# Optimization experiments

Hardware: AMD Instinct MI355X
Metric: run time of the kernel (lower is better)

## Reference

```python
import jax, jax.numpy as jnp
import numpy as np

EPS = 1e-5


def _bn_relu(y, g, beta, relu=True):
    # BatchNorm1d in training mode: biased batch stats over (B, V) per channel
    mean = jnp.mean(y, axis=(0, 2), keepdims=True)
    var = jnp.mean((y - mean) ** 2, axis=(0, 2), keepdims=True)
    out = (y - mean) * jax.lax.rsqrt(var + EPS) * g[None, :, None] + beta[None, :, None]
    return jnp.maximum(out, 0.0) if relu else out


def _spiral_conv(x, idx, w, b, g, beta):
    # x: (B,C,V), idx: (V,L) -> gather (B,C,V,L), row-major reshape to (B,C*L,V)
    B, C, V = x.shape
    L = idx.shape[1]
    neigh = x[:, :, idx].reshape(B, C * L, V)
    y = jnp.einsum('om,bmv->bov', w, neigh) + b[None, :, None]
    return _bn_relu(y, g, beta)


def _se(x, w1, w2):
    s = jnp.mean(x, axis=2)                              # (B,C)
    h = jnp.maximum(jnp.einsum('bc,rc->br', s, w1), 0.0)  # (B,r)
    s = jax.nn.sigmoid(jnp.einsum('br,cr->bc', h, w2))   # (B,C)
    return x * s[:, :, None]


def setup_inputs() -> dict:
    key = jax.random.key(0)
    ks = jax.random.split(key, 24)
    B, V, L, H = 2, 16384, 12, 256
    sc = 0.05
    inp = {
        'verts': jax.random.normal(ks[0], (B, V, 3), jnp.float32),
        'spirals': jax.random.randint(ks[1], (4, V, L), 0, V, jnp.int32),
        'enc0_w': jax.random.normal(ks[2], (H, 3 * L), jnp.float32) * sc,
        'enc0_b': jax.random.normal(ks[3], (H,), jnp.float32) * sc,
        'enc0_g': jnp.ones((H,), jnp.float32),
        'enc0_beta': jnp.zeros((H,), jnp.float32),
        'enc_w': jax.random.normal(ks[4], (3, H, H * L), jnp.float32) * sc,
        'enc_b': jax.random.normal(ks[5], (3, H), jnp.float32) * sc,
        'enc_g': jnp.ones((3, H), jnp.float32),
        'enc_beta': jnp.zeros((3, H), jnp.float32),
        'se_w1': jax.random.normal(ks[6], (4, H // 8, H), jnp.float32) * sc,
        'se_w2': jax.random.normal(ks[7], (4, H, H // 8), jnp.float32) * sc,
        'skip_w': jax.random.normal(ks[8], (3, H, 2 * H), jnp.float32) * sc,
        'skip_b': jax.random.normal(ks[9], (3, H), jnp.float32) * sc,
        'dec_w': jax.random.normal(ks[10], (3, H, H * L), jnp.float32) * sc,
        'dec_b': jax.random.normal(ks[11], (3, H), jnp.float32) * sc,
        'dec_g': jnp.ones((3, H), jnp.float32),
        'dec_beta': jnp.zeros((3, H), jnp.float32),
        'cls1_w': jax.random.normal(ks[12], (H // 2, H), jnp.float32) * sc,
        'cls1_b': jax.random.normal(ks[13], (H // 2,), jnp.float32) * sc,
        'cls1_g': jnp.ones((H // 2,), jnp.float32),
        'cls1_beta': jnp.zeros((H // 2,), jnp.float32),
        'cls2_w': jax.random.normal(ks[14], (H // 4, H // 2), jnp.float32) * sc,
        'cls2_b': jax.random.normal(ks[15], (H // 4,), jnp.float32) * sc,
        'cls2_g': jnp.ones((H // 4,), jnp.float32),
        'cls2_beta': jnp.zeros((H // 4,), jnp.float32),
        'cls3_w': jax.random.normal(ks[16], (1, H // 4), jnp.float32) * sc,
        'cls3_b': jax.random.normal(ks[17], (1,), jnp.float32) * sc,
    }
    return inp


def reference(verts, spirals, enc0_w, enc0_b, enc0_g, enc0_beta,
              enc_w, enc_b, enc_g, enc_beta, se_w1, se_w2,
              skip_w, skip_b, dec_w, dec_b, dec_g, dec_beta,
              cls1_w, cls1_b, cls1_g, cls1_beta,
              cls2_w, cls2_b, cls2_g, cls2_beta, cls3_w, cls3_b):
    x = jnp.transpose(verts, (0, 2, 1))  # (B,3,V)
    feats = []
    # encoder: 4 blocks, block0 has no residual (3 != 256)
    for i in range(4):
        if i == 0:
            out = _spiral_conv(x, spirals[0], enc0_w, enc0_b, enc0_g, enc0_beta)
        else:
            out = _spiral_conv(x, spirals[i], enc_w[i - 1], enc_b[i - 1], enc_g[i - 1], enc_beta[i - 1]) + x
        x = _se(out, se_w1[i], se_w2[i])
        feats.append(x)
    # decoder with skip-concat fusion, spirals[2],[1],[0] and feats[2],[1],[0]
    for i in range(3):
        feat = feats[2 - i]
        idx = spirals[2 - i]
        xc = jnp.concatenate([x, feat], axis=1)  # (B,512,V)
        x = jnp.einsum('oc,bcv->bov', skip_w[i], xc) + skip_b[i][None, :, None]
        x = _spiral_conv(x, idx, dec_w[i], dec_b[i], dec_g[i], dec_beta[i]) + x
    # classifier: 1x1 conv stack
    h = _bn_relu(jnp.einsum('oc,bcv->bov', cls1_w, x) + cls1_b[None, :, None], cls1_g, cls1_beta)
    h = _bn_relu(jnp.einsum('oc,bcv->bov', cls2_w, h) + cls2_b[None, :, None], cls2_g, cls2_beta)
    out = jnp.einsum('oc,bcv->bov', cls3_w, h) + cls3_b[None, :, None]  # (B,1,V)
    return out[:, 0, :]  # (B,V)
```

## Files before the change

kernel.cpp:

```cpp
#include <hip/hip_runtime.h>

typedef unsigned short u16;
using f16x8 = __attribute__((ext_vector_type(8))) _Float16;
using f32x4 = __attribute__((ext_vector_type(4))) float;

#define V_N 16384
#define M_N 32768

__device__ __forceinline__ float h2f(u16 u) {
  _Float16 h; __builtin_memcpy(&h, &u, 2); return (float)h;
}
__device__ __forceinline__ u16 f2h(float f) {
  _Float16 h = (_Float16)f; u16 u; __builtin_memcpy(&u, &h, 2); return u;
}

__device__ __forceinline__ void dma16(const u16* g, u16* l) {
  __builtin_amdgcn_global_load_lds(
      (const __attribute__((address_space(1))) void*)(const void*)g,
      (__attribute__((address_space(3))) void*)(void*)l, 16, 0, 0);
}

__device__ __forceinline__ void d_perm2(int bid, const float* __restrict__ w, u16* __restrict__ wp) {
  int o = bid & 255, layer = bid >> 8;
  int t = threadIdx.x;
  const float* src = w + ((size_t)layer * 256 + o) * 3072;
  u16* dst = wp + (size_t)layer * 786432;
  float2 v[6];
  #pragma unroll
  for (int q = 0; q < 6; ++q) v[q] = *(const float2*)(src + t * 12 + q * 2);
  const float* vf = (const float*)v;
  int lo = t & 31;
  #pragma unroll
  for (int m = 0; m < 12; ++m) {
    int kc = m * 8 + (t >> 5);
    dst[(size_t)kc * 8192 + o * 32 + lo] = f2h(vf[m]);
  }
}

__device__ __forceinline__ void d_permfr(int bid, const float* __restrict__ src, u16* __restrict__ dst,
                                         int O, int K) {
  int i = bid * 256 + threadIdx.x;
  if (i >= (K << 8)) return;
  int j = i & 7, lq = (i >> 3) & 3, col = (i >> 5) & 255, kc = i >> 13;
  int k = kc * 32 + lq * 8 + j;
  float v = (col < O) ? src[(size_t)col * K + k] : 0.f;
  dst[i] = f2h(v);
}

__global__ __launch_bounds__(256) void prep_k(
    const float* __restrict__ enc_w, const float* __restrict__ dec_w,
    const float* __restrict__ skip_w, const float* __restrict__ cls1_w,
    const float* __restrict__ cls2_w,
    u16* __restrict__ wpe, u16* __restrict__ wpe_dec, u16* __restrict__ skip_wb,
    u16* __restrict__ cls1_wb, u16* __restrict__ wp6, float* __restrict__ zbase)
{
  int b = blockIdx.x;
  if (b < 768) { d_perm2(b, enc_w, wpe); return; }
  b -= 768;
  if (b < 768) { d_perm2(b, dec_w, wpe_dec); return; }
  b -= 768;
  if (b < 1536) {
    int s = b >> 9, r = b & 511;
    d_permfr(r, skip_w + (size_t)s * 256 * 512, skip_wb + (size_t)s * 256 * 512, 256, 512);
    return;
  }
  b -= 1536;
  if (b < 256) { d_permfr(b, cls1_w, cls1_wb, 128, 256); return; }
  b -= 256;
  if (b < 128) { d_permfr(b, cls2_w, wp6, 64, 128); return; }
  b -= 128;
  int idx = (b * 256 + threadIdx.x) * 2;
  if (idx < 7168) { zbase[idx] = 0.f; zbase[idx + 1] = 0.f; }
}

__global__ __launch_bounds__(256) void wscale_k(const u16* __restrict__ w, const float* __restrict__ sig,
                                                const float* __restrict__ sigx,
                                                u16* __restrict__ o, int n, int sel) {
  int i = blockIdx.x * 256 + threadIdx.x;
  if (i >= n) return;
  float wv = h2f(w[i]);
  int k = (i >> 13) * 32 + ((i >> 3) & 3) * 8 + (i & 7);
  int c = k & 255;
  #pragma unroll
  for (int b = 0; b < 2; ++b) {
    float s;
    if (sel == 511 && k < 256) s = sigx ? sigx[b * 256 + c] : 1.f;
    else                       s = sig[b * 256 + c];
    o[(long)b * n + i] = f2h(wv * s);
  }
}

__global__ __launch_bounds__(256) void enc0_k(const float* __restrict__ verts, const int* __restrict__ sp,
                                              const float* __restrict__ w0, u16* __restrict__ y,
                                              float* __restrict__ st) {
  __shared__ float xs[32][36];
  int t = threadIdx.x;
  int r0 = blockIdx.x * 32;
  for (int s = t; s < 32 * 12; s += 256) {
    int row = s / 12, tt = s - row * 12;
    int gr = r0 + row;
    int b = gr >> 14, v = gr & (V_N - 1);
    int j = sp[tt * V_N + v];
    const float* p = verts + ((long)b * V_N + j) * 3;
    xs[row][tt]      = p[0];
    xs[row][12 + tt] = p[1];
    xs[row][24 + tt] = p[2];
  }
  __syncthreads();
  float w[36];
  #pragma unroll
  for (int k = 0; k < 36; ++k) w[k] = w0[t * 36 + k];
  float s1 = 0.f, s2 = 0.f;
  for (int row = 0; row < 32; ++row) {
    float a = 0.f;
    #pragma unroll
    for (int k = 0; k < 36; ++k) a += w[k] * xs[row][k];
    u16 h = f2h(a);
    y[(long)(r0 + row) * 256 + t] = h;
    float av = h2f(h);
    s1 += av; s2 += av * av;
  }
  atomicAdd(&st[t], s1);
  atomicAdd(&st[256 + t], s2);
}

template<int CT>
__global__ __launch_bounds__(512, 4) void gemm3_k(
    const u16* __restrict__ P0, const u16* __restrict__ P1, int lda,
    const int* __restrict__ sp, int L,
    const u16* __restrict__ Wt, long wstride,
    u16* __restrict__ Yb, const float* __restrict__ bias, int Ostore,
    float* __restrict__ stats)
{
  constexpr int KC   = CT >> 5;
  constexpr int PH   = (CT == 256) ? 4 : 2;
  constexpr int KCP  = KC / PH;
  constexpr int PROW = 64;
  constexpr int BUFE = 64 * PROW;
  __shared__ __align__(16) u16 lA[3 * BUFE];
  const int tid  = threadIdx.x;
  const int wave = tid >> 6, lane = tid & 63;
  const int wn = wave * 32;
  const int lr = lane & 15, lq = lane >> 4;
  const int nwg = gridDim.x;
  const int wg = (blockIdx.x & 7) * (nwg >> 3) + (blockIdx.x >> 3);
  const int bm = wg * 64;
  const int batch = bm >> 14;
  const int vbase = bm & (V_N - 1);
  const int qrow = lane >> 3;
  const int qchunk = lane & 7;
  const bool gat = (sp != nullptr);
  const long rowb = (long)batch * V_N;
  const u16* Pd1 = P1 ? P1 : P0;
  const u16* Wb = Wt + (long)batch * wstride;
  const int NS = PH * L;

  const u16* bp[2];
  #pragma unroll
  for (int nt = 0; nt < 2; ++nt)
    bp[nt] = Wb + ((long)(wn + nt * 16 + lr) * 4 + lq) * 8;

  const u16* aBase[4][2];
  #pragma unroll
  for (int mt = 0; mt < 4; ++mt)
    #pragma unroll
    for (int kp = 0; kp < 2; ++kp) {
      int row = mt * 16 + lr;
      aBase[mt][kp] = lA + row * PROW + (((kp * 4 + lq) ^ (row & 7)) << 3);
    }

  auto load_idx = [&](int tap) -> int {
    int v = 0;
    if (gat && lane < 8) v = sp[(long)tap * V_N + vbase + wave * 8 + lane];
    return v;
  };

  auto dma_st = [&](u16* buf, const u16* src, int idxreg, int ph) {
    u16* wb = buf + wave * (8 * PROW);
    int rloc = wave * 8 + qrow;
    long grow;
    if (gat) grow = rowb + (long)__shfl(idxreg, qrow, 64);
    else     grow = bm + rloc;
    const u16* gp = src + grow * lda + ph * PROW + ((qchunk ^ (rloc & 7)) << 3);
    dma16(gp, wb);
  };

  f32x4 acc[4][2];
  #pragma unroll
  for (int i = 0; i < 4; ++i)
    #pragma unroll
    for (int j = 0; j < 2; ++j) acc[i][j] = (f32x4){0.f, 0.f, 0.f, 0.f};

  f16x8 tA[KCP * 2], tB2[KCP * 2];

  auto adv = [&](int& l, int& ph) { if (++l == L) { l = 0; ++ph; } };
  int lB = 0, phB = 0; adv(lB, phB);
  int lD = lB, phD = phB; adv(lD, phD);
  int lI = lD; { int pT = phD; int lT = lI; adv(lT, pT); lI = lT; }
  int idxN;

  {
    int i0 = load_idx(0);
    int i1 = load_idx(lB);
    idxN = load_idx(lD);
    dma_st(lA, P0, i0, 0);
    if (NS > 1) {
      const u16* s1 = (!gat && lB > 0) ? Pd1 : P0;
      dma_st(lA + BUFE, s1, i1, phB);
    }
    __builtin_amdgcn_sched_barrier(0);
    #pragma unroll
    for (int kp = 0; kp < KCP; ++kp)
      #pragma unroll
      for (int nt = 0; nt < 2; ++nt)
        tA[kp * 2 + nt] = *(const f16x8*)(bp[nt] + (long)kp * 8192);
    __builtin_amdgcn_sched_barrier(0);
  }

  auto stage = [&](int s, f16x8 (&tCur)[KCP * 2], f16x8 (&tNxt)[KCP * 2]) {
    if (s + 1 < NS) asm volatile("s_waitcnt vmcnt(5)" ::: "memory");
    else            asm volatile("s_waitcnt vmcnt(0)" ::: "memory");
    asm volatile("s_waitcnt lgkmcnt(0)" ::: "memory");
    __builtin_amdgcn_s_barrier();
    __builtin_amdgcn_sched_barrier(0);
    const int so = (s % 3) * BUFE;
    const long cbB = (long)(lB * KC + phB * KCP);
    f16x8 a0[4];
    #pragma unroll
    for (int mt = 0; mt < 4; ++mt) a0[mt] = *(const f16x8*)(aBase[mt][0] + so);
    if (s + 1 < NS) {
      tNxt[0] = *(const f16x8*)(bp[0] + cbB * 8192);
      tNxt[1] = *(const f16x8*)(bp[1] + cbB * 8192);
    }
    __builtin_amdgcn_sched_barrier(0);
    __builtin_amdgcn_s_setprio(1);
    #pragma unroll
    for (int mt = 0; mt < 4; ++mt) {
      acc[mt][0] = __builtin_amdgcn_mfma_f32_16x16x32_f16(a0[mt], tCur[0], acc[mt][0], 0, 0, 0);
      acc[mt][1] = __builtin_amdgcn_mfma_f32_16x16x32_f16(a0[mt], tCur[1], acc[mt][1], 0, 0, 0);
    }
    __builtin_amdgcn_s_setprio(0);
    __builtin_amdgcn_sched_barrier(0);
    int idxT = 0;
    if (gat && s + 3 < NS) idxT = load_idx(lI);
    if (s + 2 < NS) {
      const u16* srcD = (!gat && lD > 0) ? Pd1 : P0;
      dma_st(lA + ((s + 2) % 3) * BUFE, srcD, idxN, phD);
    }
    __builtin_amdgcn_sched_barrier(0);
    f16x8 a1[4];
    #pragma unroll
    for (int mt = 0; mt < 4; ++mt) a1[mt] = *(const f16x8*)(aBase[mt][1] + so);
    if (s + 1 < NS) {
      tNxt[2] = *(const f16x8*)(bp[0] + (cbB + 1) * 8192);
      tNxt[3] = *(const f16x8*)(bp[1] + (cbB + 1) * 8192);
    }
    __builtin_amdgcn_sched_barrier(0);
    __builtin_amdgcn_s_setprio(1);
    #pragma unroll
    for (int mt = 0; mt < 4; ++mt) {
      acc[mt][0] = __builtin_amdgcn_mfma_f32_16x16x32_f16(a1[mt], tCur[2], acc[mt][0], 0, 0, 0);
      acc[mt][1] = __builtin_amdgcn_mfma_f32_16x16x32_f16(a1[mt], tCur[3], acc[mt][1], 0, 0, 0);
    }
    __builtin_amdgcn_s_setprio(0);
    adv(lB, phB); adv(lD, phD); if (++lI == L) lI = 0;
    idxN = idxT;
  };

  for (int s = 0; s < NS; s += 2) {
    stage(s, tA, tB2);
    stage(s + 1, tB2, tA);
  }

  #pragma unroll
  for (int nt = 0; nt < 2; ++nt) {
    int col = wn + nt * 16 + lr;
    if (col < Ostore) {
      float bv = bias ? bias[col] : 0.f;
      float s1 = 0.f, s2 = 0.f;
      #pragma unroll
      for (int mt = 0; mt < 4; ++mt) {
        #pragma unroll
        for (int rg = 0; rg < 4; ++rg) {
          int row = bm + mt * 16 + lq * 4 + rg;
          float v = acc[mt][nt][rg] + bv;
          Yb[(long)row * Ostore + col] = f2h(v);
          s1 += v; s2 += v * v;
        }
      }
      if (stats) {
        s1 += __shfl_xor(s1, 16); s1 += __shfl_xor(s1, 32);
        s2 += __shfl_xor(s2, 16); s2 += __shfl_xor(s2, 32);
        if (lq == 0) {
          atomicAdd(&stats[col], s1);
          atomicAdd(&stats[Ostore + col], s2);
        }
      }
    }
  }
}

__global__ __launch_bounds__(256) void bnrelu2_k(
    const u16* __restrict__ y, const float* __restrict__ st,
    const float* __restrict__ g, const float* __restrict__ be,
    const u16* __restrict__ resid, const float* __restrict__ rscale,
    u16* __restrict__ ob, float* __restrict__ ses, int O)
{
  __shared__ float sL[256];
  int tid = threadIdx.x;
  int tpr = O >> 2;
  int rpi = 256 / tpr;
  int ci = (tid & (tpr - 1)) * 4;
  int row0 = blockIdx.x * (rpi * 16);
  int r0 = row0 + (tid / tpr);
  int b = row0 >> 14;
  float mean[4], sc[4], sh[4], rs[4];
  #pragma unroll
  for (int j = 0; j < 4; ++j) {
    int c = ci + j;
    float m = st[c] * (1.f / 32768.f);
    float var = st[O + c] * (1.f / 32768.f) - m * m;
    mean[j] = m;
    sc[j] = rsqrtf(fmaxf(var, 0.f) + 1e-5f) * g[c];
    sh[j] = be[c];
    rs[j] = rscale ? rscale[b * 256 + c] : 1.f;
  }
  float ss[4] = {0,0,0,0};
  for (int it = 0; it < 16; ++it) {
    long i = ((long)r0 + (long)it * rpi) * O + ci;
    uint2 pv = *(const uint2*)(y + i);
    float v[4];
    v[0] = fmaxf((h2f((u16)(pv.x & 0xffff)) - mean[0]) * sc[0] + sh[0], 0.f);
    v[1] = fmaxf((h2f((u16)(pv.x >> 16))    - mean[1]) * sc[1] + sh[1], 0.f);
    v[2] = fmaxf((h2f((u16)(pv.y & 0xffff)) - mean[2]) * sc[2] + sh[2], 0.f);
    v[3] = fmaxf((h2f((u16)(pv.y >> 16))    - mean[3]) * sc[3] + sh[3], 0.f);
    if (resid) {
      uint2 rv = *(const uint2*)(resid + i);
      v[0] += h2f((u16)(rv.x & 0xffff)) * rs[0]; v[1] += h2f((u16)(rv.x >> 16)) * rs[1];
      v[2] += h2f((u16)(rv.y & 0xffff)) * rs[2]; v[3] += h2f((u16)(rv.y >> 16)) * rs[3];
    }
    uint2 pk;
    pk.x = (unsigned)f2h(v[0]) | ((unsigned)f2h(v[1]) << 16);
    pk.y = (unsigned)f2h(v[2]) | ((unsigned)f2h(v[3]) << 16);
    *(uint2*)(ob + i) = pk;
    #pragma unroll
    for (int j = 0; j < 4; ++j) ss[j] += v[j];
  }
  if (ses) {
    sL[tid] = 0.f;
    __syncthreads();
    #pragma unroll
    for (int j = 0; j < 4; ++j) atomicAdd(&sL[ci + j], ss[j]);
    __syncthreads();
    atomicAdd(&ses[b * O + tid], sL[tid]);
  }
}

__global__ void se_k(const float* __restrict__ ses, const float* __restrict__ w1,
                     const float* __restrict__ w2, float* __restrict__ sig)
{
  __shared__ float s[256];
  __shared__ float h[32];
  int b = blockIdx.x, t = threadIdx.x;
  s[t] = ses[b * 256 + t] * (1.f / 16384.f);
  __syncthreads();
  if (t < 32) {
    float a = 0.f;
    for (int c = 0; c < 256; ++c) a += w1[t * 256 + c] * s[c];
    h[t] = fmaxf(a, 0.f);
  }
  __syncthreads();
  float a = 0.f;
  #pragma unroll
  for (int r = 0; r < 32; ++r) a += w2[t * 32 + r] * h[r];
  sig[b * 256 + t] = 1.f / (1.f + expf(-a));
}

__global__ __launch_bounds__(256) void cls3_k(const u16* __restrict__ h2, const float* __restrict__ w,
                                              const float* __restrict__ b, float* __restrict__ out)
{
  __shared__ float ws[64];
  int t = threadIdx.x;
  if (t < 64) ws[t] = w[t];
  __syncthreads();
  int r = blockIdx.x * 256 + t;
  const u16* p = h2 + (long)r * 64;
  float a = b[0];
  #pragma unroll
  for (int c = 0; c < 64; ++c) a += ws[c] * h2f(p[c]);
  out[r] = a;
}

extern "C" void kernel_launch(void* const* d_in, const int* in_sizes, int n_in,
                              void* d_out, int out_size, void* d_ws, size_t ws_size,
                              hipStream_t stream)
{
  (void)in_sizes; (void)n_in; (void)out_size; (void)ws_size;
  const float* verts   = (const float*)d_in[0];
  const int*   spirals = (const int*)d_in[1];
  const float* enc0_w  = (const float*)d_in[2];
  const float* enc0_g  = (const float*)d_in[4];
  const float* enc0_be = (const float*)d_in[5];
  const float* enc_w   = (const float*)d_in[6];
  const float* enc_g   = (const float*)d_in[8];
  const float* enc_be  = (const float*)d_in[9];
  const float* se_w1   = (const float*)d_in[10];
  const float* se_w2   = (const float*)d_in[11];
  const float* skip_w  = (const float*)d_in[12];
  const float* skip_b  = (const float*)d_in[13];
  const float* dec_w   = (const float*)d_in[14];
  const float* dec_g   = (const float*)d_in[16];
  const float* dec_be  = (const float*)d_in[17];
  const float* cls1_w  = (const float*)d_in[18];
  const float* cls1_g  = (const float*)d_in[20];
  const float* cls1_be = (const float*)d_in[21];
  const float* cls2_w  = (const float*)d_in[22];
  const float* cls2_g  = (const float*)d_in[24];
  const float* cls2_be = (const float*)d_in[25];
  const float* cls3_w  = (const float*)d_in[26];
  const float* cls3_b  = (const float*)d_in[27];

  char* p = (char*)d_ws;
  auto alloc = [&](size_t n) { char* q = p; p += (n + 255) & ~(size_t)255; return q; };
  u16* wpe     = (u16*)alloc((size_t)6 * 256 * 3072 * 2);
  u16* wpe_s   = (u16*)alloc((size_t)3 * 2 * 256 * 3072 * 2);
  u16* skip_wb = (u16*)alloc((size_t)3 * 256 * 512 * 2);
  u16* skip_s  = (u16*)alloc((size_t)3 * 2 * 256 * 512 * 2);
  u16* cls1_wb = (u16*)alloc((size_t)256 * 256 * 2);
  u16* wp6     = (u16*)alloc((size_t)256 * 128 * 2);
  float* stats = (float*)alloc(10 * 2048);
  float* sesum = (float*)alloc(4 * 2048);
  float* sig   = (float*)alloc(4 * 2048);
  u16* out0 = (u16*)alloc((size_t)M_N * 256 * 2);
  u16* out1 = (u16*)alloc((size_t)M_N * 256 * 2);
  u16* out2 = (u16*)alloc((size_t)M_N * 256 * 2);
  u16* ct   = (u16*)alloc((size_t)M_N * 256 * 2);
  u16* tb   = (u16*)alloc((size_t)M_N * 256 * 2);
  u16* xd   = (u16*)alloc((size_t)M_N * 256 * 2);
  u16* outs[4] = {out0, out1, out2, ct};
  const size_t WENC = (size_t)256 * 3072;
  const size_t WSKP = (size_t)256 * 512;

  prep_k<<<3472, 256, 0, stream>>>(enc_w, dec_w, skip_w, cls1_w, cls2_w,
                                   wpe, wpe + (size_t)3 * WENC, skip_wb, cls1_wb, wp6,
                                   stats);

  enc0_k<<<1024, 256, 0, stream>>>(verts, spirals, enc0_w, ct, stats);
  bnrelu2_k<<<512, 256, 0, stream>>>(ct, stats, enc0_g, enc0_be, nullptr, nullptr, out0, sesum, 256);
  se_k<<<2, 256, 0, stream>>>(sesum, se_w1, se_w2, sig);

  for (int i = 1; i < 4; ++i) {
    wscale_k<<<3072, 256, 0, stream>>>(wpe + (size_t)(i - 1) * WENC, sig + (i - 1) * 512, nullptr,
                                       wpe_s + (size_t)(i - 1) * 2 * WENC, (int)WENC, 255);
    gemm3_k<256><<<512, 512, 0, stream>>>(outs[i - 1], nullptr, 256,
                                          spirals + (size_t)i * V_N * 12, 12,
                                          wpe_s + (size_t)(i - 1) * 2 * WENC, (long)WENC,
                                          ct, nullptr, 256, stats + i * 512);
    bnrelu2_k<<<512, 256, 0, stream>>>(ct, stats + i * 512, enc_g + (i - 1) * 256, enc_be + (i - 1) * 256,
                                       outs[i - 1], sig + (i - 1) * 512, outs[i], sesum + i * 512, 256);
    se_k<<<2, 256, 0, stream>>>(sesum + i * 512, se_w1 + (size_t)i * 32 * 256,
                                se_w2 + (size_t)i * 256 * 32, sig + i * 512);
  }

  for (int i = 0; i < 3; ++i) {
    wscale_k<<<512, 256, 0, stream>>>(skip_wb + (size_t)i * WSKP, sig + (2 - i) * 512,
                                      (i == 0) ? (sig + 3 * 512) : nullptr,
                                      skip_s + (size_t)i * 2 * WSKP, (int)WSKP, 511);
    gemm3_k<256><<<512, 512, 0, stream>>>((i == 0) ? ct : xd, outs[2 - i], 256, nullptr, 2,
                                          skip_s + (size_t)i * 2 * WSKP, (long)WSKP,
                                          tb, skip_b + i * 256, 256, nullptr);
    gemm3_k<256><<<512, 512, 0, stream>>>(tb, nullptr, 256,
                                          spirals + (size_t)(2 - i) * V_N * 12, 12,
                                          wpe + (size_t)(3 + i) * WENC, 0,
                                          outs[2 - i], nullptr, 256, stats + (4 + i) * 512);
    bnrelu2_k<<<512, 256, 0, stream>>>(outs[2 - i], stats + (4 + i) * 512, dec_g + i * 256, dec_be + i * 256,
                                       tb, nullptr, xd, nullptr, 256);
  }

  gemm3_k<256><<<512, 512, 0, stream>>>(xd, nullptr, 256, nullptr, 1,
                                        cls1_wb, 0, ct, nullptr, 128, stats + 7 * 512);
  bnrelu2_k<<<256, 256, 0, stream>>>(ct, stats + 7 * 512, cls1_g, cls1_be, nullptr, nullptr,
                                     ct, nullptr, 128);
  gemm3_k<128><<<512, 512, 0, stream>>>(ct, nullptr, 128, nullptr, 1,
                                        wp6, 0, tb, nullptr, 64, stats + 8 * 512);
  bnrelu2_k<<<128, 256, 0, stream>>>(tb, stats + 8 * 512, cls2_g, cls2_be, nullptr, nullptr,
                                     tb, nullptr, 64);
  cls3_k<<<128, 256, 0, stream>>>(tb, cls3_w, cls3_b, (float*)d_out);
}
```

Baseline: 868.6 us.

## Fold SE gate computation into consumers and fuse final classifier into BN kernel

Removes the standalone SE gate kernel and the final 1x1 classifier kernel. Each wscale and bnrelu block now recomputes the squeeze-excite gate from the channel sums in shared memory, and the last BN+ReLU pass does the 64-wide dot product with a shuffle reduction and writes the output directly. The aim is fewer launches and one less round trip of the hidden activations through memory. The cost is redundant gate work in every block: 3072 blocks for the encoder wscale each run a small MLP with several barriers, which could outweigh the launch savings.

Result: slower. 1.013 ms (+16.6%).

```diff
diff --git a/kernel.cpp b/kernel.cpp
--- a/kernel.cpp
+++ b/kernel.cpp
@@ -18,6 +18,36 @@
   __builtin_amdgcn_global_load_lds(
       (const __attribute__((address_space(1))) void*)(const void*)g,
       (__attribute__((address_space(3))) void*)(void*)l, 16, 0, 0);
+}
+
+__device__ __forceinline__ float gate256(const float* __restrict__ ses_b,
+                                         const float* __restrict__ w1,
+                                         const float* __restrict__ w2,
+                                         float* sL, float* h8, float* hL, int t)
+{
+  sL[t] = ses_b[t] * (1.f / 16384.f);
+  __syncthreads();
+  {
+    int r = t >> 3, gseg = t & 7;
+    const float* wr = w1 + r * 256 + gseg * 32;
+    const float* sv = sL + gseg * 32;
+    float a = 0.f;
+    #pragma unroll
+    for (int c = 0; c < 32; ++c) a += wr[c] * sv[c];
+    h8[t] = a;
+  }
+  __syncthreads();
+  if (t < 32) {
+    float a = 0.f;
+    #pragma unroll
+    for (int j = 0; j < 8; ++j) a += h8[t * 8 + j];
+    hL[t] = fmaxf(a, 0.f);
+  }
+  __syncthreads();
+  float a = 0.f;
+  #pragma unroll
+  for (int r = 0; r < 32; ++r) a += w2[t * 32 + r] * hL[r];
+  return 1.f / (1.f + expf(-a));
 }
 
 __device__ __forceinline__ void d_perm2(int bid, const float* __restrict__ w, u16* __restrict__ wp) {
@@ -73,19 +103,39 @@
   if (idx < 7168) { zbase[idx] = 0.f; zbase[idx + 1] = 0.f; }
 }
 
-__global__ __launch_bounds__(256) void wscale_k(const u16* __restrict__ w, const float* __restrict__ sig,
-                                                const float* __restrict__ sigx,
-                                                u16* __restrict__ o, int n, int sel) {
-  int i = blockIdx.x * 256 + threadIdx.x;
-  if (i >= n) return;
+__global__ __launch_bounds__(256) void wscale_k(
+    const u16* __restrict__ w,
+    const float* __restrict__ ses, const float* __restrict__ w1, const float* __restrict__ w2,
+    const float* __restrict__ sesx, const float* __restrict__ x1, const float* __restrict__ x2,
+    u16* __restrict__ o, int n, int sel)
+{
+  __shared__ float sL[256], h8[256], hL[32];
+  __shared__ float gA[512], gX[512];
+  int t = threadIdx.x;
+  #pragma unroll
+  for (int b = 0; b < 2; ++b) {
+    float v = gate256(ses + b * 256, w1, w2, sL, h8, hL, t);
+    __syncthreads();
+    gA[b * 256 + t] = v;
+  }
+  if (sesx) {
+    #pragma unroll
+    for (int b = 0; b < 2; ++b) {
+      float v = gate256(sesx + b * 256, x1, x2, sL, h8, hL, t);
+      __syncthreads();
+      gX[b * 256 + t] = v;
+    }
+  }
+  __syncthreads();
+  int i = blockIdx.x * 256 + t;
   float wv = h2f(w[i]);
   int k = (i >> 13) * 32 + ((i >> 3) & 3) * 8 + (i & 7);
   int c = k & 255;
   #pragma unroll
   for (int b = 0; b < 2; ++b) {
     float s;
-    if (sel == 511 && k < 256) s = sigx ? sigx[b * 256 + c] : 1.f;
-    else                       s = sig[b * 256 + c];
+    if (sel == 511 && k < 256) s = sesx ? gX[b * 256 + c] : 1.f;
+    else                       s = gA[b * 256 + c];
     o[(long)b * n + i] = f2h(wv * s);
   }
 }
@@ -303,10 +353,12 @@
 __global__ __launch_bounds__(256) void bnrelu2_k(
     const u16* __restrict__ y, const float* __restrict__ st,
     const float* __restrict__ g, const float* __restrict__ be,
-    const u16* __restrict__ resid, const float* __restrict__ rscale,
-    u16* __restrict__ ob, float* __restrict__ ses, int O)
+    const u16* __restrict__ resid,
+    const float* __restrict__ pses, const float* __restrict__ pw1, const float* __restrict__ pw2,
+    u16* __restrict__ ob, float* __restrict__ ses, int O,
+    const float* __restrict__ w3, const float* __restrict__ b3, float* __restrict__ outp)
 {
-  __shared__ float sL[256];
+  __shared__ float sL[256], h8[256], hL[32];
   int tid = threadIdx.x;
   int tpr = O >> 2;
   int rpi = 256 / tpr;
@@ -314,7 +366,17 @@
   int row0 = blockIdx.x * (rpi * 16);
   int r0 = row0 + (tid / tpr);
   int b = row0 >> 14;
-  float mean[4], sc[4], sh[4], rs[4];
+  float rs[4] = {1.f, 1.f, 1.f, 1.f};
+  if (resid && pses) {
+    float v = gate256(pses + b * 256, pw1, pw2, sL, h8, hL, tid);
+    __syncthreads();
+    h8[tid] = v;
+    __syncthreads();
+    #pragma unroll
+    for (int j = 0; j < 4; ++j) rs[j] = h8[ci + j];
+    __syncthreads();
+  }
+  float mean[4], sc[4], sh[4];
   #pragma unroll
   for (int j = 0; j < 4; ++j) {
     int c = ci + j;
@@ -323,11 +385,17 @@
     mean[j] = m;
     sc[j] = rsqrtf(fmaxf(var, 0.f) + 1e-5f) * g[c];
     sh[j] = be[c];
-    rs[j] = rscale ? rscale[b * 256 + c] : 1.f;
+  }
+  float w3v[4]; float b3v = 0.f;
+  if (w3) {
+    #pragma unroll
+    for (int j = 0; j < 4; ++j) w3v[j] = w3[ci + j];
+    b3v = b3[0];
   }
   float ss[4] = {0,0,0,0};
   for (int it = 0; it < 16; ++it) {
-    long i = ((long)r0 + (long)it * rpi) * O + ci;
+    int r = r0 + it * rpi;
+    long i = (long)r * O + ci;
     uint2 pv = *(const uint2*)(y + i);
     float v[4];
     v[0] = fmaxf((h2f((u16)(pv.x & 0xffff)) - mean[0]) * sc[0] + sh[0], 0.f);
@@ -339,10 +407,17 @@
       v[0] += h2f((u16)(rv.x & 0xffff)) * rs[0]; v[1] += h2f((u16)(rv.x >> 16)) * rs[1];
       v[2] += h2f((u16)(rv.y & 0xffff)) * rs[2]; v[3] += h2f((u16)(rv.y >> 16)) * rs[3];
     }
-    uint2 pk;
-    pk.x = (unsigned)f2h(v[0]) | ((unsigned)f2h(v[1]) << 16);
-    pk.y = (unsigned)f2h(v[2]) | ((unsigned)f2h(v[3]) << 16);
-    *(uint2*)(ob + i) = pk;
+    if (w3) {
+      float pr = w3v[0] * v[0] + w3v[1] * v[1] + w3v[2] * v[2] + w3v[3] * v[3];
+      pr += __shfl_xor(pr, 1); pr += __shfl_xor(pr, 2);
+      pr += __shfl_xor(pr, 4); pr += __shfl_xor(pr, 8);
+      if ((tid & 15) == 0) outp[(long)r] = pr + b3v;
+    } else {
+      uint2 pk;
+      pk.x = (unsigned)f2h(v[0]) | ((unsigned)f2h(v[1]) << 16);
+      pk.y = (unsigned)f2h(v[2]) | ((unsigned)f2h(v[3]) << 16);
+      *(uint2*)(ob + i) = pk;
+    }
     #pragma unroll
     for (int j = 0; j < 4; ++j) ss[j] += v[j];
   }
@@ -354,41 +429,6 @@
     __syncthreads();
     atomicAdd(&ses[b * O + tid], sL[tid]);
   }
-}
-
-__global__ void se_k(const float* __restrict__ ses, const float* __restrict__ w1,
-                     const float* __restrict__ w2, float* __restrict__ sig)
-{
-  __shared__ float s[256];
-  __shared__ float h[32];
-  int b = blockIdx.x, t = threadIdx.x;
-  s[t] = ses[b * 256 + t] * (1.f / 16384.f);
-  __syncthreads();
-  if (t < 32) {
-    float a = 0.f;
-    for (int c = 0; c < 256; ++c) a += w1[t * 256 + c] * s[c];
-    h[t] = fmaxf(a, 0.f);
-  }
-  __syncthreads();
-  float a = 0.f;
-  #pragma unroll
-  for (int r = 0; r < 32; ++r) a += w2[t * 32 + r] * h[r];
-  sig[b * 256 + t] = 1.f / (1.f + expf(-a));
-}
-
-__global__ __launch_bounds__(256) void cls3_k(const u16* __restrict__ h2, const float* __restrict__ w,
-                                              const float* __restrict__ b, float* __restrict__ out)
-{
-  __shared__ float ws[64];
-  int t = threadIdx.x;
-  if (t < 64) ws[t] = w[t];
-  __syncthreads();
-  int r = blockIdx.x * 256 + t;
-  const u16* p = h2 + (long)r * 64;
-  float a = b[0];
-  #pragma unroll
-  for (int c = 0; c < 64; ++c) a += ws[c] * h2f(p[c]);
-  out[r] = a;
 }
 
 extern "C" void kernel_launch(void* const* d_in, const int* in_sizes, int n_in,
@@ -430,7 +470,6 @@
   u16* wp6     = (u16*)alloc((size_t)256 * 128 * 2);
   float* stats = (float*)alloc(10 * 2048);
   float* sesum = (float*)alloc(4 * 2048);
-  float* sig   = (float*)alloc(4 * 2048);
   u16* out0 = (u16*)alloc((size_t)M_N * 256 * 2);
   u16* out1 = (u16*)alloc((size_t)M_N * 256 * 2);
   u16* out2 = (u16*)alloc((size_t)M_N * 256 * 2);
@@ -440,31 +479,38 @@
   u16* outs[4] = {out0, out1, out2, ct};
   const size_t WENC = (size_t)256 * 3072;
   const size_t WSKP = (size_t)256 * 512;
+  const size_t SEW = (size_t)32 * 256;
 
   prep_k<<<3472, 256, 0, stream>>>(enc_w, dec_w, skip_w, cls1_w, cls2_w,
                                    wpe, wpe + (size_t)3 * WENC, skip_wb, cls1_wb, wp6,
                                    stats);
 
   enc0_k<<<1024, 256, 0, stream>>>(verts, spirals, enc0_w, ct, stats);
-  bnrelu2_k<<<512, 256, 0, stream>>>(ct, stats, enc0_g, enc0_be, nullptr, nullptr, out0, sesum, 256);
-  se_k<<<2, 256, 0, stream>>>(sesum, se_w1, se_w2, sig);
+  bnrelu2_k<<<512, 256, 0, stream>>>(ct, stats, enc0_g, enc0_be, nullptr,
+                                     nullptr, nullptr, nullptr, out0, sesum, 256,
+                                     nullptr, nullptr, nullptr);
 
   for (int i = 1; i < 4; ++i) {
-    wscale_k<<<3072, 256, 0, stream>>>(wpe + (size_t)(i - 1) * WENC, sig + (i - 1) * 512, nullptr,
+    wscale_k<<<3072, 256, 0, stream>>>(wpe + (size_t)(i - 1) * WENC,
+                                       sesum + (i - 1) * 512, se_w1 + (i - 1) * SEW, se_w2 + (i - 1) * SEW,
+                                       nullptr, nullptr, nullptr,
                                        wpe_s + (size_t)(i - 1) * 2 * WENC, (int)WENC, 255);
     gemm3_k<256><<<512, 512, 0, stream>>>(outs[i - 1], nullptr, 256,
                                           spirals + (size_t)i * V_N * 12, 12,
                                           wpe_s + (size_t)(i - 1) * 2 * WENC, (long)WENC,
                                           ct, nullptr, 256, stats + i * 512);
     bnrelu2_k<<<512, 256, 0, stream>>>(ct, stats + i * 512, enc_g + (i - 1) * 256, enc_be + (i - 1) * 256,
-                                       outs[i - 1], sig + (i - 1) * 512, outs[i], sesum + i * 512, 256);
-    se_k<<<2, 256, 0, stream>>>(sesum + i * 512, se_w1 + (size_t)i * 32 * 256,
-                                se_w2 + (size_t)i * 256 * 32, sig + i * 512);
+                                       outs[i - 1],
+                                       sesum + (i - 1) * 512, se_w1 + (i - 1) * SEW, se_w2 + (i - 1) * SEW,
+                                       outs[i], sesum + i * 512, 256,
+                                       nullptr, nullptr, nullptr);
   }
 
   for (int i = 0; i < 3; ++i) {
-    wscale_k<<<512, 256, 0, stream>>>(skip_wb + (size_t)i * WSKP, sig + (2 - i) * 512,
-                                      (i == 0) ? (sig + 3 * 512) : nullptr,
+    wscale_k<<<512, 256, 0, stream>>>(skip_wb + (size_t)i * WSKP,
+                                      sesum + (2 - i) * 512, se_w1 + (2 - i) * SEW, se_w2 + (2 - i) * SEW,
+                                      (i == 0) ? (sesum + 3 * 512) : nullptr,
+                                      se_w1 + 3 * SEW, se_w2 + 3 * SEW,
                                       skip_s + (size_t)i * 2 * WSKP, (int)WSKP, 511);
     gemm3_k<256><<<512, 512, 0, stream>>>((i == 0) ? ct : xd, outs[2 - i], 256, nullptr, 2,
                                           skip_s + (size_t)i * 2 * WSKP, (long)WSKP,
@@ -474,16 +520,18 @@
                                           wpe + (size_t)(3 + i) * WENC, 0,
                                           outs[2 - i], nullptr, 256, stats + (4 + i) * 512);
     bnrelu2_k<<<512, 256, 0, stream>>>(outs[2 - i], stats + (4 + i) * 512, dec_g + i * 256, dec_be + i * 256,
-                                       tb, nullptr, xd, nullptr, 256);
+                                       tb, nullptr, nullptr, nullptr,
+                                       xd, nullptr, 256, nullptr, nullptr, nullptr);
   }
 
   gemm3_k<256><<<512, 512, 0, stream>>>(xd, nullptr, 256, nullptr, 1,
                                         cls1_wb, 0, ct, nullptr, 128, stats + 7 * 512);
-  bnrelu2_k<<<256, 256, 0, stream>>>(ct, stats + 7 * 512, cls1_g, cls1_be, nullptr, nullptr,
-                                     ct, nullptr, 128);
+  bnrelu2_k<<<256, 256, 0, stream>>>(ct, stats + 7 * 512, cls1_g, cls1_be, nullptr,
+                                     nullptr, nullptr, nullptr, ct, nullptr, 128,
+                                     nullptr, nullptr, nullptr);
   gemm3_k<128><<<512, 512, 0, stream>>>(ct, nullptr, 128, nullptr, 1,
                                         wp6, 0, tb, nullptr, 64, stats + 8 * 512);
-  bnrelu2_k<<<128, 256, 0, stream>>>(tb, stats + 8 * 512, cls2_g, cls2_be, nullptr, nullptr,
-                                     tb, nullptr, 64);
-  cls3_k<<<128, 256, 0, stream>>>(tb, cls3_w, cls3_b, (float*)d_out);
-}
+  bnrelu2_k<<<128, 256, 0, stream>>>(tb, stats + 8 * 512, cls2_g, cls2_be, nullptr,
+                                     nullptr, nullptr, nullptr, tb, nullptr, 64,
+                                     cls3_w, cls3_b, (float*)d_out);
+}
```
